# Optimization experiments

Hardware: AMD Instinct MI355X
Metric: run time of the kernel (lower is better)

## Reference

```python
import jax, jax.numpy as jnp
import numpy as np

H = 48; W = 48; WS = 8; NH = 12; FTH = 0.4; EPS = 1e-6


def _layernorm(x, w, b):
    mu = jnp.mean(x, axis=-1, keepdims=True)
    var = jnp.mean((x - mu) ** 2, axis=-1, keepdims=True)
    return (x - mu) * jax.lax.rsqrt(var + EPS) * w + b


def _mha(x, w_qkv, b_qkv, w_o, b_o, key_mask=None):
    # x: (Bn, N, C); w_qkv: (3, C, C); key_mask: (Bn, N) bool or None
    Bn, N, C = x.shape
    d = C // NH
    qkv = jnp.einsum('bnc,tcd->tbnd', x, w_qkv) + b_qkv[:, None, None, :]
    q, k, v = [t.reshape(Bn, N, NH, d).transpose(0, 2, 1, 3) for t in qkv]
    s = jnp.einsum('bhqd,bhkd->bhqk', q, k) / jnp.sqrt(jnp.asarray(d, x.dtype))
    if key_mask is not None:
        s = jnp.where(key_mask[:, None, None, :], s, jnp.asarray(-1e9, s.dtype))
    p = jax.nn.softmax(s, axis=-1)
    ctx = jnp.einsum('bhqk,bhkd->bhqd', p, v).transpose(0, 2, 1, 3).reshape(Bn, N, C)
    return ctx @ w_o + b_o


def _forward(x, mask, w_qkv_g, b_qkv_g, w_o_g, b_o_g, w_qkv_l, b_qkv_l, w_o_l, b_o_l,
             ln1_w, ln1_b, ln2_w, ln2_b, w_fc1, b_fc1, w_fc2, b_fc2):
    B, L, C = x.shape
    shortcut = x
    xn = _layernorm(x, ln1_w, ln1_b)

    # avg_pool2d(mask, 4, 4) -> (B, H, W); fg/bg split
    pooled = mask.reshape(B, 1, H, 4, W, 4).mean(axis=(3, 5))[:, 0]      # (B,H,W)
    fg = pooled > FTH                                                    # bool (B,H,W)
    fg_tok = fg.reshape(B, L)
    bg = (~fg).astype(x.dtype)
    # window-level bg mask: avg_pool(bg, WS) > 0 -> window contains any bg token
    bg_win = bg.reshape(B, H // WS, WS, W // WS, WS).mean(axis=(2, 4)) > 0.0   # (B, nH, nW)
    bg_win_tok = jnp.broadcast_to(bg_win[:, :, None, :, None],
                                  (B, H // WS, WS, W // WS, WS)).reshape(B, L)

    # local windowed attention on all windows (equivalent on bg windows; masked out elsewhere)
    xw = xn.reshape(B, H // WS, WS, W // WS, WS, C).transpose(0, 1, 3, 2, 4, 5)
    xw = xw.reshape(-1, WS * WS, C)                                      # (B*nWin, WS*WS, C)
    lout = _mha(xw, w_qkv_l, b_qkv_l, w_o_l, b_o_l)
    lout = lout.reshape(B, H // WS, W // WS, WS, WS, C).transpose(0, 1, 3, 2, 4, 5)
    lout = lout.reshape(B, L, C)

    # global attention with fg key mask (fg queries attend fg keys only)
    gout = _mha(xn, w_qkv_g, b_qkv_g, w_o_g, b_o_g, key_mask=fg_tok)

    # scatter-back semantics: fg positions take global output; bg-window positions take local output; rest zero
    zero = jnp.zeros((), x.dtype)
    x_new = jnp.where(fg_tok[..., None], gout,
                      jnp.where(bg_win_tok[..., None], lout, zero))

    x1 = shortcut + x_new
    h = _layernorm(x1, ln2_w, ln2_b)
    h = jax.nn.gelu(h @ w_fc1 + b_fc1, approximate=False) @ w_fc2 + b_fc2
    return x1 + h


def setup_inputs() -> dict:
    key = jax.random.key(0)
    ks = jax.random.split(key, 8)
    B, L, C, M = 2, H * W, 768, 3072
    s = 0.02
    return {
        'x': jax.random.normal(ks[0], (B, L, C), jnp.float32),
        'mask': jax.random.uniform(ks[1], (B, 1, 4 * H, 4 * W), jnp.float32),
        'w_qkv_g': jax.random.normal(ks[2], (3, C, C), jnp.float32) * s,
        'b_qkv_g': jnp.zeros((3, C), jnp.float32),
        'w_o_g': jax.random.normal(ks[3], (C, C), jnp.float32) * s,
        'b_o_g': jnp.zeros((C,), jnp.float32),
        'w_qkv_l': jax.random.normal(ks[4], (3, C, C), jnp.float32) * s,
        'b_qkv_l': jnp.zeros((3, C), jnp.float32),
        'w_o_l': jax.random.normal(ks[5], (C, C), jnp.float32) * s,
        'b_o_l': jnp.zeros((C,), jnp.float32),
        'ln1_w': jnp.ones((C,), jnp.float32),
        'ln1_b': jnp.zeros((C,), jnp.float32),
        'ln2_w': jnp.ones((C,), jnp.float32),
        'ln2_b': jnp.zeros((C,), jnp.float32),
        'w_fc1': jax.random.normal(ks[6], (C, M), jnp.float32) * s,
        'b_fc1': jnp.zeros((M,), jnp.float32),
        'w_fc2': jax.random.normal(ks[7], (M, C), jnp.float32) * s,
        'b_fc2': jnp.zeros((C,), jnp.float32),
    }


def reference(x, mask, w_qkv_g, b_qkv_g, w_o_g, b_o_g, w_qkv_l, b_qkv_l, w_o_l, b_o_l,
              ln1_w, ln1_b, ln2_w, ln2_b, w_fc1, b_fc1, w_fc2, b_fc2):
    return _forward(x, mask, w_qkv_g, b_qkv_g, w_o_g, b_o_g, w_qkv_l, b_qkv_l, w_o_l, b_o_l,
                    ln1_w, ln1_b, ln2_w, ln2_b, w_fc1, b_fc1, w_fc2, b_fc2)
```

## Files before the change

### kernel.cpp

```cpp
#include <hip/hip_runtime.h>
#include <math.h>

#define Lh 2304
#define Ch 768
#define NHh 12
#define Bh 2
#define QS2 3072

typedef unsigned short ushort_t;
typedef unsigned int uint_t;
typedef __attribute__((ext_vector_type(8))) short bf16x8;
typedef __attribute__((ext_vector_type(4))) float f32x4;
#define MFMA16(a, b, c) __builtin_amdgcn_mfma_f32_16x16x32_bf16(a, b, c, 0, 0, 0)

#define SCL2 0.18033688f
#define MSK2 1.4426950e9f
#if __has_builtin(__builtin_amdgcn_exp2f)
#define EXP2F(x) __builtin_amdgcn_exp2f(x)
#else
#define EXP2F(x) exp2f(x)
#endif

__device__ __forceinline__ ushort_t f2bf(float f) {
    union { float f; uint_t u; } v; v.f = f;
    uint_t u = v.u + 0x7fffu + ((v.u >> 16) & 1u);
    return (ushort_t)(u >> 16);
}
__device__ __forceinline__ uint_t pack2bf(float a, float b) {
    return (uint_t)f2bf(a) | ((uint_t)f2bf(b) << 16);
}

__device__ __forceinline__ void llds16(ushort_t* dst, const ushort_t* src) {
    __builtin_amdgcn_global_load_lds(
        (__attribute__((address_space(1))) void*)(const_cast<ushort_t*>(src)),
        (__attribute__((address_space(3))) void*)dst, 16, 0, 0);
}

__device__ __forceinline__ void ln_body(const float* __restrict__ x, const float* __restrict__ w,
                                        const float* __restrict__ b, ushort_t* __restrict__ y,
                                        int row, float* red)
{
    int tid = threadIdx.x;
    const float* xr = x + (size_t)row * Ch;
    float v0 = xr[tid], v1 = xr[tid + 256], v2 = xr[tid + 512];
    red[tid] = v0 + v1 + v2;
    __syncthreads();
    for (int st = 128; st > 0; st >>= 1) {
        if (tid < st) red[tid] += red[tid + st];
        __syncthreads();
    }
    float mean = red[0] * (1.0f / 768.0f);
    __syncthreads();
    float d0 = v0 - mean, d1 = v1 - mean, d2 = v2 - mean;
    red[tid] = d0 * d0 + d1 * d1 + d2 * d2;
    __syncthreads();
    for (int st = 128; st > 0; st >>= 1) {
        if (tid < st) red[tid] += red[tid + st];
        __syncthreads();
    }
    float rstd = rsqrtf(red[0] * (1.0f / 768.0f) + 1e-6f);
    ushort_t* yr = y + (size_t)row * Ch;
    yr[tid]       = f2bf(d0 * rstd * w[tid]       + b[tid]);
    yr[tid + 256] = f2bf(d1 * rstd * w[tid + 256] + b[tid + 256]);
    yr[tid + 512] = f2bf(d2 * rstd * w[tid + 512] + b[tid + 512]);
}

__global__ __launch_bounds__(256)
void layernorm_bf16_kernel(const float* __restrict__ x, const float* __restrict__ w,
                           const float* __restrict__ b, ushort_t* __restrict__ y)
{
    __shared__ float red[256];
    ln_body(x, w, b, y, blockIdx.x, red);
}

__global__ __launch_bounds__(256)
void ln_mask_kernel(const float* __restrict__ x, const float* __restrict__ w,
                    const float* __restrict__ b, ushort_t* __restrict__ y,
                    const float* __restrict__ mask, float* __restrict__ fg,
                    float* __restrict__ bgw)
{
    __shared__ float red[256];
    int bid = blockIdx.x;
    if (bid < 4608) {
        ln_body(x, w, b, y, bid, red);
        return;
    }
    int win = bid - 4608;
    int tid = threadIdx.x;
    if (tid >= 64) return;
    int bb = win / 36, ww = win % 36;
    int wi = ww / 6, wj = ww % 6;
    int i = wi * 8 + (tid >> 3), j = wj * 8 + (tid & 7);
    const float* mb = mask + (size_t)bb * 192 * 192 + (size_t)(i * 4) * 192 + j * 4;
    float s = 0.0f;
    #pragma unroll
    for (int di = 0; di < 4; ++di) {
        float4 v = *(const float4*)(mb + (size_t)di * 192);
        s += v.x + v.y + v.z + v.w;
    }
    float f = (s * (1.0f / 16.0f) > 0.4f) ? 1.0f : 0.0f;
    fg[bb * Lh + i * 48 + j] = f;
    unsigned long long bg = __ballot(f == 0.0f);
    if (tid == 0) bgw[win] = bg ? 1.0f : 0.0f;
}

__global__ __launch_bounds__(256)
void transpose_all_kernel(const float* __restrict__ w_qkv_g, const float* __restrict__ w_qkv_l,
                          const float* __restrict__ w_o_g, const float* __restrict__ w_o_l,
                          const float* __restrict__ w_fc1, const float* __restrict__ w_fc2,
                          const float* __restrict__ b_qkv_g, const float* __restrict__ b_qkv_l,
                          ushort_t* __restrict__ wtq, ushort_t* __restrict__ wt_o_g,
                          ushort_t* __restrict__ wt_o_l, ushort_t* __restrict__ wt_fc1,
                          ushort_t* __restrict__ wt_fc2, float* __restrict__ biasq)
{
    int blk = blockIdx.x;
    int tid = threadIdx.x;
    if (blk >= 2304) {
        int which = blk - 2304;
        const float* src = which ? b_qkv_l : b_qkv_g;
        float* dst = biasq + which * 2304;
        for (int i = tid; i < 2304; i += 256) dst[i] = src[i];
        return;
    }
    const float* W; ushort_t* D; int K, N, nx, bx;
    const size_t CC = (size_t)Ch * Ch;
    if (blk < 432)       { int t = blk / 144; bx = blk % 144;
                           W = w_qkv_g + t * CC; D = wtq + t * CC; K = 768; N = 768; nx = 12; }
    else if (blk < 864)  { int r = blk - 432; int t = r / 144; bx = r % 144;
                           W = w_qkv_l + t * CC; D = wtq + (size_t)2304 * 768 + t * CC;
                           K = 768; N = 768; nx = 12; }
    else if (blk < 1008) { bx = blk - 864;  W = w_o_g; D = wt_o_g; K = 768; N = 768; nx = 12; }
    else if (blk < 1152) { bx = blk - 1008; W = w_o_l; D = wt_o_l; K = 768; N = 768; nx = 12; }
    else if (blk < 1728) { bx = blk - 1152; W = w_fc1; D = wt_fc1; K = 768; N = 3072; nx = 48; }
    else                 { bx = blk - 1728; W = w_fc2; D = wt_fc2; K = 3072; N = 768; nx = 12; }
    int n0 = (bx % nx) * 64;
    int k0 = (bx / nx) * 64;
    __shared__ float T[64][65];
    #pragma unroll
    for (int i = 0; i < 16; ++i) {
        int lin = i * 256 + tid;
        int r = lin >> 6, c = lin & 63;
        T[r][c] = W[(size_t)(k0 + r) * N + n0 + c];
    }
    __syncthreads();
    #pragma unroll
    for (int i = 0; i < 4; ++i) {
        int lin = i * 256 + tid;
        int r = lin >> 4, c0 = (lin & 15) * 4;
        uint_t lo = pack2bf(T[c0][r], T[c0 + 1][r]);
        uint_t hi = pack2bf(T[c0 + 2][r], T[c0 + 3][r]);
        *(uint2*)&D[(size_t)(n0 + r) * K + k0 + c0] = make_uint2(lo, hi);
    }
}

template<int BNt, int VMODE>
__global__ __launch_bounds__(256)
void gemm_bf16_t(const ushort_t* __restrict__ A, const ushort_t* __restrict__ Bt,
                 const float* __restrict__ bias, const float* __restrict__ residual,
                 void* __restrict__ C, ushort_t* __restrict__ vt,
                 int M, int N, int K, int flags)
{
    __shared__ ushort_t AsL[2][128 * 32];
    __shared__ ushort_t BsL[2][BNt * 32];
    int bm = blockIdx.y * 128;
    int bx = blockIdx.x;
    int bn;
    if (VMODE == 1) {
        bn = (bx < 6) ? 1536 + bx * 128 : 3840 + (bx - 6) * 128;
    } else if (flags & 4) {
        bn = (bx < 12) ? bx * 128 : 2304 + (bx - 12) * 128;
    } else {
        bn = bx * BNt;
    }
    int tid = threadIdx.x;
    int lane = tid & 63;
    int wave = tid >> 6;
    int wm = wave >> 1, wn = wave & 1;
    int quad = lane >> 4, l15 = lane & 15;
    constexpr int NJ = BNt / 32;

    int srow = lane >> 2;
    int sg8 = ((lane & 3) ^ ((lane >> 3) & 3)) * 8;
    int fsw = (l15 >> 1) & 3;

    f32x4 acc[4][NJ];
    #pragma unroll
    for (int i = 0; i < 4; ++i)
        #pragma unroll
        for (int j = 0; j < NJ; ++j)
            acc[i][j] = (f32x4){0.f, 0.f, 0.f, 0.f};

    int iters = K / 32;
    llds16(&AsL[0][wave * 512], A + (size_t)(bm + wave * 16 + srow) * K + sg8);
    llds16(&AsL[0][(wave + 4) * 512], A + (size_t)(bm + (wave + 4) * 16 + srow) * K + sg8);
    llds16(&BsL[0][wave * 512], Bt + (size_t)(bn + wave * 16 + srow) * K + sg8);
    if (BNt == 128)
        llds16(&BsL[0][(wave + 4) * 512], Bt + (size_t)(bn + (wave + 4) * 16 + srow) * K + sg8);

    for (int kt = 0; kt < iters; ++kt) {
        int cur = kt & 1;
        __syncthreads();

        bf16x8 af[4], bfr[NJ];
        #pragma unroll
        for (int i = 0; i < 4; ++i)
            af[i] = *(const bf16x8*)&AsL[cur][(wm * 64 + i * 16 + l15) * 32 + ((quad ^ fsw) * 8)];
        #pragma unroll
        for (int j = 0; j < NJ; ++j)
            bfr[j] = *(const bf16x8*)&BsL[cur][(wn * (BNt / 2) + j * 16 + l15) * 32 + ((quad ^ fsw) * 8)];

        if (kt + 1 < iters) {
            int k0 = (kt + 1) * 32;
            int nxt = 1 - cur;
            llds16(&AsL[nxt][wave * 512], A + (size_t)(bm + wave * 16 + srow) * K + k0 + sg8);
            llds16(&AsL[nxt][(wave + 4) * 512], A + (size_t)(bm + (wave + 4) * 16 + srow) * K + k0 + sg8);
            llds16(&BsL[nxt][wave * 512], Bt + (size_t)(bn + wave * 16 + srow) * K + k0 + sg8);
            if (BNt == 128)
                llds16(&BsL[nxt][(wave + 4) * 512], Bt + (size_t)(bn + (wave + 4) * 16 + srow) * K + k0 + sg8);
        }

        if constexpr (VMODE == 0) {
            #pragma unroll
            for (int i = 0; i < 4; ++i)
                #pragma unroll
                for (int j = 0; j < NJ; ++j)
                    acc[i][j] = MFMA16(bfr[j], af[i], acc[i][j]);
        } else {
            #pragma unroll
            for (int i = 0; i < 4; ++i)
                #pragma unroll
                for (int j = 0; j < NJ; ++j)
                    acc[i][j] = MFMA16(af[i], bfr[j], acc[i][j]);
        }
    }

    if constexpr (VMODE == 1) {
        #pragma unroll
        for (int j = 0; j < NJ; ++j) {
            int col = bn + wn * (BNt / 2) + j * 16 + l15;
            int colp = col - ((col >= 3840) ? 3072 : 1536);
            float bc = bias[col];
            #pragma unroll
            for (int i = 0; i < 4; ++i) {
                int row0 = bm + wm * 64 + i * 16 + quad * 4;
                *(uint2*)&vt[(size_t)colp * 4608 + row0] =
                    make_uint2(pack2bf(acc[i][j][0] + bc, acc[i][j][1] + bc),
                               pack2bf(acc[i][j][2] + bc, acc[i][j][3] + bc));
            }
        }
        return;
    }

    #pragma unroll
    for (int i = 0; i < 4; ++i) {
        int row = bm + wm * 64 + i * 16 + l15;
        #pragma unroll
        for (int j = 0; j < NJ; ++j) {
            int col = bn + wn * (BNt / 2) + j * 16 + quad * 4;
            float4 bia = *(const float4*)&bias[col];
            float o0 = acc[i][j][0] + bia.x;
            float o1 = acc[i][j][1] + bia.y;
            float o2 = acc[i][j][2] + bia.z;
            float o3 = acc[i][j][3] + bia.w;
            if (flags & 1) {
                o0 = o0 * 0.5f * (1.0f + erff(o0 * 0.70710678f));
                o1 = o1 * 0.5f * (1.0f + erff(o1 * 0.70710678f));
                o2 = o2 * 0.5f * (1.0f + erff(o2 * 0.70710678f));
                o3 = o3 * 0.5f * (1.0f + erff(o3 * 0.70710678f));
            }
            if (residual) {
                float4 rs = *(const float4*)&residual[(size_t)row * N + col];
                o0 += rs.x; o1 += rs.y; o2 += rs.z; o3 += rs.w;
            }
            if (flags & 4) {
                int cq = col - ((col >= 2304) ? 768 : 0);
                *(uint2*)&((ushort_t*)C)[(size_t)row * QS2 + cq] =
                    make_uint2(pack2bf(o0, o1), pack2bf(o2, o3));
            } else if (flags & 2) {
                *(uint2*)&((ushort_t*)C)[(size_t)row * N + col] =
                    make_uint2(pack2bf(o0, o1), pack2bf(o2, o3));
            } else {
                *(float4*)&((float*)C)[(size_t)row * N + col] =
                    make_float4(o0, o1, o2, o3);
            }
        }
    }
}

__global__ __launch_bounds__(256)
void oproj_dual_kernel(const ushort_t* __restrict__ ctxg, const ushort_t* __restrict__ ctxl,
                       const ushort_t* __restrict__ Wg, const ushort_t* __restrict__ Wl,
                       const float* __restrict__ biasg, const float* __restrict__ biasl,
                       const float* __restrict__ x, float* __restrict__ x1,
                       const float* __restrict__ fg, const float* __restrict__ bgw)
{
    __shared__ ushort_t AgL[2][128 * 32];
    __shared__ ushort_t AlL[2][128 * 32];
    __shared__ ushort_t BgL[2][64 * 32];
    __shared__ ushort_t BlL[2][64 * 32];
    int bm = blockIdx.y * 128;
    int bn = blockIdx.x * 64;
    int tid = threadIdx.x;
    int lane = tid & 63;
    int wave = tid >> 6;
    int wm = wave >> 1, wn = wave & 1;
    int quad = lane >> 4, l15 = lane & 15;

    int srow = lane >> 2;
    int sg8 = ((lane & 3) ^ ((lane >> 3) & 3)) * 8;
    int fsw = (l15 >> 1) & 3;
    const int K = Ch, N = Ch, iters = Ch / 32;

    f32x4 accg[4][2], accl[4][2];
    #pragma unroll
    for (int i = 0; i < 4; ++i)
        #pragma unroll
        for (int j = 0; j < 2; ++j) {
            accg[i][j] = (f32x4){0.f, 0.f, 0.f, 0.f};
            accl[i][j] = (f32x4){0.f, 0.f, 0.f, 0.f};
        }

    llds16(&AgL[0][wave * 512], ctxg + (size_t)(bm + wave * 16 + srow) * K + sg8);
    llds16(&AgL[0][(wave + 4) * 512], ctxg + (size_t)(bm + (wave + 4) * 16 + srow) * K + sg8);
    llds16(&AlL[0][wave * 512], ctxl + (size_t)(bm + wave * 16 + srow) * K + sg8);
    llds16(&AlL[0][(wave + 4) * 512], ctxl + (size_t)(bm + (wave + 4) * 16 + srow) * K + sg8);
    llds16(&BgL[0][wave * 512], Wg + (size_t)(bn + wave * 16 + srow) * K + sg8);
    llds16(&BlL[0][wave * 512], Wl + (size_t)(bn + wave * 16 + srow) * K + sg8);

    for (int kt = 0; kt < iters; ++kt) {
        int cur = kt & 1;
        __syncthreads();
        bf16x8 afg[4], afl[4], bfg[2], bfl[2];
        #pragma unroll
        for (int i = 0; i < 4; ++i) {
            afg[i] = *(const bf16x8*)&AgL[cur][(wm * 64 + i * 16 + l15) * 32 + ((quad ^ fsw) * 8)];
            afl[i] = *(const bf16x8*)&AlL[cur][(wm * 64 + i * 16 + l15) * 32 + ((quad ^ fsw) * 8)];
        }
        #pragma unroll
        for (int j = 0; j < 2; ++j) {
            bfg[j] = *(const bf16x8*)&BgL[cur][(wn * 32 + j * 16 + l15) * 32 + ((quad ^ fsw) * 8)];
            bfl[j] = *(const bf16x8*)&BlL[cur][(wn * 32 + j * 16 + l15) * 32 + ((quad ^ fsw) * 8)];
        }
        if (kt + 1 < iters) {
            int k0 = (kt + 1) * 32;
            int nxt = 1 - cur;
            llds16(&AgL[nxt][wave * 512], ctxg + (size_t)(bm + wave * 16 + srow) * K + k0 + sg8);
            llds16(&AgL[nxt][(wave + 4) * 512], ctxg + (size_t)(bm + (wave + 4) * 16 + srow) * K + k0 + sg8);
            llds16(&AlL[nxt][wave * 512], ctxl + (size_t)(bm + wave * 16 + srow) * K + k0 + sg8);
            llds16(&AlL[nxt][(wave + 4) * 512], ctxl + (size_t)(bm + (wave + 4) * 16 + srow) * K + k0 + sg8);
            llds16(&BgL[nxt][wave * 512], Wg + (size_t)(bn + wave * 16 + srow) * K + k0 + sg8);
            llds16(&BlL[nxt][wave * 512], Wl + (size_t)(bn + wave * 16 + srow) * K + k0 + sg8);
        }
        #pragma unroll
        for (int i = 0; i < 4; ++i)
            #pragma unroll
            for (int j = 0; j < 2; ++j)
                accg[i][j] = MFMA16(bfg[j], afg[i], accg[i][j]);
        #pragma unroll
        for (int i = 0; i < 4; ++i)
            #pragma unroll
            for (int j = 0; j < 2; ++j)
                accl[i][j] = MFMA16(bfl[j], afl[i], accl[i][j]);
    }

    #pragma unroll
    for (int i = 0; i < 4; ++i) {
        int row = bm + wm * 64 + i * 16 + l15;
        int bb = (row >= Lh) ? 1 : 0;
        int n = row - bb * Lh;
        int ii = n / 48, jj = n % 48;
        float keepg = (fg[row] != 0.0f) ? 1.0f : 0.0f;
        float keepl = (keepg == 0.0f &&
                       bgw[bb * 36 + (ii >> 3) * 6 + (jj >> 3)] != 0.0f) ? 1.0f : 0.0f;
        #pragma unroll
        for (int j = 0; j < 2; ++j) {
            int col = bn + wn * 32 + j * 16 + quad * 4;
            float4 bg4 = *(const float4*)&biasg[col];
            float4 bl4 = *(const float4*)&biasl[col];
            float4 x4 = *(const float4*)&x[(size_t)row * N + col];
            float4 o;
            o.x = x4.x + keepg * (accg[i][j][0] + bg4.x) + keepl * (accl[i][j][0] + bl4.x);
            o.y = x4.y + keepg * (accg[i][j][1] + bg4.y) + keepl * (accl[i][j][1] + bl4.y);
            o.z = x4.z + keepg * (accg[i][j][2] + bg4.z) + keepl * (accl[i][j][2] + bl4.z);
            o.w = x4.w + keepg * (accg[i][j][3] + bg4.w) + keepl * (accl[i][j][3] + bl4.w);
            *(float4*)&x1[(size_t)row * N + col] = o;
        }
    }
}

__device__ __forceinline__ void attn_global_body(
    const ushort_t* __restrict__ QKV, const ushort_t* __restrict__ VT,
    const float* __restrict__ fg,
    float* __restrict__ Opart, float* __restrict__ Lpart,
    int tile, int h, int b, int half,
    ushort_t (*Ks)[2][64][32], ushort_t (*Vs)[2][64][32],
    ushort_t (*Ps)[72], float (*fgs)[64])
{
    int tid = threadIdx.x;
    int lane = tid & 63;
    int wave = tid >> 6;
    int quad = lane >> 4, l15 = lane & 15;
    int kb0 = half * 1152;

    bf16x8 aq[2][2];
    #pragma unroll
    for (int s = 0; s < 2; ++s) {
        int tok = tile * 128 + wave * 32 + s * 16 + l15;
        const ushort_t* qbase = QKV + (size_t)(b * Lh + tok) * QS2 + h * 64;
        #pragma unroll
        for (int step = 0; step < 2; ++step)
            aq[s][step] = *(const bf16x8*)(qbase + step * 32 + quad * 8);
    }

    int srow = lane >> 2;
    int sc = lane & 3;
    int krow = wave * 16 + srow;
    int scx = (sc ^ ((krow >> 1) & 3)) * 8;
    const ushort_t* ksrc = QKV + (size_t)(b * Lh + kb0 + krow) * QS2 + 768 + h * 64 + scx;
    const ushort_t* vsrc = VT + (size_t)(h * 64 + krow) * 4608 + b * Lh + kb0 + scx;

    float l_part[2] = {0.f, 0.f};
    f32x4 o_acc[2][4];
    #pragma unroll
    for (int s = 0; s < 2; ++s)
        #pragma unroll
        for (int t4 = 0; t4 < 4; ++t4) o_acc[s][t4] = (f32x4){0.f, 0.f, 0.f, 0.f};

    llds16(&Ks[0][0][wave * 16][0], ksrc);
    llds16(&Ks[0][1][wave * 16][0], ksrc + 32);
    llds16(&Vs[0][0][wave * 16][0], vsrc);
    llds16(&Vs[0][1][wave * 16][0], vsrc + 32);
    if (tid < 64) fgs[0][tid] = (fg[b * Lh + kb0 + tid] - 1.0f) * MSK2;

    int rfs = (l15 >> 1) & 3;

    for (int kt = 0; kt < 18; ++kt) {
        int cur = kt & 1, nxt = cur ^ 1;
        __syncthreads();

        bf16x8 bk[2][4];
        #pragma unroll
        for (int step = 0; step < 2; ++step)
            #pragma unroll
            for (int j4 = 0; j4 < 4; ++j4)
                bk[step][j4] = *(const bf16x8*)&Ks[cur][step][j4 * 16 + l15][(quad ^ rfs) * 8];

        if (kt + 1 < 18) {
            const ushort_t* kp = ksrc + (size_t)(kt + 1) * 64 * QS2;
            const ushort_t* vp = vsrc + (kt + 1) * 64;
            llds16(&Ks[nxt][0][wave * 16][0], kp);
            llds16(&Ks[nxt][1][wave * 16][0], kp + 32);
            llds16(&Vs[nxt][0][wave * 16][0], vp);
            llds16(&Vs[nxt][1][wave * 16][0], vp + 32);
            if (tid < 64) fgs[nxt][tid] = (fg[b * Lh + kb0 + (kt + 1) * 64 + tid] - 1.0f) * MSK2;
        }

        f32x4 s4[2][4];
        #pragma unroll
        for (int s = 0; s < 2; ++s)
            #pragma unroll
            for (int j4 = 0; j4 < 4; ++j4) s4[s][j4] = (f32x4){0.f, 0.f, 0.f, 0.f};
        __builtin_amdgcn_s_setprio(1);
        #pragma unroll
        for (int step = 0; step < 2; ++step)
            #pragma unroll
            for (int s = 0; s < 2; ++s)
                #pragma unroll
                for (int j4 = 0; j4 < 4; ++j4)
                    s4[s][j4] = MFMA16(bk[step][j4], aq[s][step], s4[s][j4]);
        __builtin_amdgcn_s_setprio(0);

        #pragma unroll
        for (int s = 0; s < 2; ++s) {
            int p0 = wave * 32 + s * 16;
            #pragma unroll
            for (int j4 = 0; j4 < 4; ++j4) {
                float4 mb4 = *(const float4*)&fgs[cur][j4 * 16 + quad * 4];
                float e0 = EXP2F(s4[s][j4][0] * SCL2 + mb4.x);
                float e1 = EXP2F(s4[s][j4][1] * SCL2 + mb4.y);
                float e2 = EXP2F(s4[s][j4][2] * SCL2 + mb4.z);
                float e3 = EXP2F(s4[s][j4][3] * SCL2 + mb4.w);
                l_part[s] += (e0 + e1) + (e2 + e3);
                uint_t a01 = __builtin_amdgcn_perm(__float_as_uint(e1), __float_as_uint(e0), 0x07060302u);
                uint_t a23 = __builtin_amdgcn_perm(__float_as_uint(e3), __float_as_uint(e2), 0x07060302u);
                *(uint2*)&Ps[p0 + l15][j4 * 16 + quad * 4] = make_uint2(a01, a23);
            }
        }
        #pragma unroll
        for (int step = 0; step < 2; ++step) {
            bf16x8 bv[4];
            #pragma unroll
            for (int t4 = 0; t4 < 4; ++t4)
                bv[t4] = *(const bf16x8*)&Vs[cur][step][t4 * 16 + l15][(quad ^ rfs) * 8];
            __builtin_amdgcn_s_setprio(1);
            #pragma unroll
            for (int s = 0; s < 2; ++s) {
                int p0 = wave * 32 + s * 16;
                bf16x8 a = *(const bf16x8*)&Ps[p0 + l15][step * 32 + quad * 8];
                #pragma unroll
                for (int t4 = 0; t4 < 4; ++t4)
                    o_acc[s][t4] = MFMA16(bv[t4], a, o_acc[s][t4]);
            }
            __builtin_amdgcn_s_setprio(0);
        }
    }

    #pragma unroll
    for (int s = 0; s < 2; ++s) {
        float v = l_part[s];
        v += __shfl_xor(v, 16, 64);
        v += __shfl_xor(v, 32, 64);
        int ql = wave * 32 + s * 16 + l15;
        int tok = tile * 128 + ql;
        float* op = Opart + ((size_t)half * 4608 + b * Lh + tok) * Ch + h * 64;
        #pragma unroll
        for (int t4 = 0; t4 < 4; ++t4)
            *(f32x4*)&op[t4 * 16 + quad * 4] = o_acc[s][t4];
        if (quad == 0)
            Lpart[((size_t)half * 4608 + b * Lh + tok) * NHh + h] = v;
    }
}

__device__ __forceinline__ void attn_local_body(
    const ushort_t* __restrict__ QKV, const ushort_t* __restrict__ VT,
    ushort_t* __restrict__ O, int tile, int h, int b,
    ushort_t (*Ks)[2][64][32], ushort_t (*Vs)[2][64][32], ushort_t (*Ps)[72])
{
    int tid = threadIdx.x;
    int lane = tid & 63;
    int wave = tid >> 6;
    int quad = lane >> 4, l15 = lane & 15;
    int wi = tile / 6, wj = tile % 6;

    bf16x8 aq[2];
    {
        int ql = wave * 16 + l15;
        int tok = (wi * 8 + (ql >> 3)) * 48 + wj * 8 + (ql & 7);
        const ushort_t* qbase = QKV + (size_t)(b * Lh + tok) * QS2 + 1536 + h * 64;
        #pragma unroll
        for (int step = 0; step < 2; ++step)
            aq[step] = *(const bf16x8*)(qbase + step * 32 + quad * 8);
    }

    {
        int srow = lane >> 2;
        int sc = lane & 3;
        int krow = wave * 16 + srow;
        int kfs = (krow >> 1) & 3;
        int tokK = (wi * 8 + (krow >> 3)) * 48 + wj * 8 + (krow & 7);
        const ushort_t* ksrc = QKV + (size_t)(b * Lh + tokK) * QS2 + 2304 + h * 64 + (sc ^ kfs) * 8;
        int c0 = sc ^ kfs;
        const ushort_t* vbase = VT + (size_t)(768 + h * 64 + krow) * 4608 + b * Lh + wj * 8;
        llds16(&Ks[0][0][wave * 16][0], ksrc);
        llds16(&Ks[0][1][wave * 16][0], ksrc + 32);
        llds16(&Vs[0][0][wave * 16][0], vbase + (wi * 8 + c0) * 48);
        llds16(&Vs[0][1][wave * 16][0], vbase + (wi * 8 + 4 + c0) * 48);
    }
    __syncthreads();

    float l_part = 0.f;
    f32x4 o_acc[4];
    #pragma unroll
    for (int t4 = 0; t4 < 4; ++t4) o_acc[t4] = (f32x4){0.f, 0.f, 0.f, 0.f};

    int rfs = (l15 >> 1) & 3;
    f32x4 s4[4];
    #pragma unroll
    for (int j4 = 0; j4 < 4; ++j4) s4[j4] = (f32x4){0.f, 0.f, 0.f, 0.f};
    #pragma unroll
    for (int step = 0; step < 2; ++step) {
        bf16x8 bk[4];
        #pragma unroll
        for (int j4 = 0; j4 < 4; ++j4)
            bk[j4] = *(const bf16x8*)&Ks[0][step][j4 * 16 + l15][(quad ^ rfs) * 8];
        #pragma unroll
        for (int j4 = 0; j4 < 4; ++j4)
            s4[j4] = MFMA16(bk[j4], aq[step], s4[j4]);
    }
    int p0 = wave * 16;
    #pragma unroll
    for (int j4 = 0; j4 < 4; ++j4) {
        float e0 = EXP2F(s4[j4][0] * SCL2);
        float e1 = EXP2F(s4[j4][1] * SCL2);
        float e2 = EXP2F(s4[j4][2] * SCL2);
        float e3 = EXP2F(s4[j4][3] * SCL2);
        l_part += (e0 + e1) + (e2 + e3);
        uint_t a01 = __builtin_amdgcn_perm(__float_as_uint(e1), __float_as_uint(e0), 0x07060302u);
        uint_t a23 = __builtin_amdgcn_perm(__float_as_uint(e3), __float_as_uint(e2), 0x07060302u);
        *(uint2*)&Ps[p0 + l15][j4 * 16 + quad * 4] = make_uint2(a01, a23);
    }
    #pragma unroll
    for (int step = 0; step < 2; ++step) {
        bf16x8 bv[4];
        #pragma unroll
        for (int t4 = 0; t4 < 4; ++t4)
            bv[t4] = *(const bf16x8*)&Vs[0][step][t4 * 16 + l15][(quad ^ rfs) * 8];
        bf16x8 a = *(const bf16x8*)&Ps[p0 + l15][step * 32 + quad * 8];
        #pragma unroll
        for (int t4 = 0; t4 < 4; ++t4)
            o_acc[t4] = MFMA16(bv[t4], a, o_acc[t4]);
    }

    {
        float v = l_part;
        v += __shfl_xor(v, 16, 64);
        v += __shfl_xor(v, 32, 64);
        float inv = 1.0f / v;
        int ql = wave * 16 + l15;
        int tok = (wi * 8 + (ql >> 3)) * 48 + wj * 8 + (ql & 7);
        ushort_t* ob = O + (size_t)(b * Lh + tok) * Ch + h * 64;
        #pragma unroll
        for (int t4 = 0; t4 < 4; ++t4) {
            *(uint2*)&ob[t4 * 16 + quad * 4] =
                make_uint2(pack2bf(o_acc[t4][0] * inv, o_acc[t4][1] * inv),
                           pack2bf(o_acc[t4][2] * inv, o_acc[t4][3] * inv));
        }
    }
}

__global__ __launch_bounds__(256)
void attn_fused_kernel(const ushort_t* __restrict__ QKV, const ushort_t* __restrict__ VT,
                       const float* __restrict__ fg,
                       float* __restrict__ Opart, float* __restrict__ Lpart,
                       ushort_t* __restrict__ ctxl)
{
    __shared__ __align__(16) ushort_t Ks[2][2][64][32];
    __shared__ __align__(16) ushort_t Vs[2][2][64][32];
    __shared__ __align__(16) ushort_t Ps[128][72];
    __shared__ float fgs[2][64];

    int bid = blockIdx.x;
    if (bid < 864) {
        int gid = (bid & 7) * 108 + (bid >> 3);
        int half = gid / 432;
        int rem = gid % 432;
        int tile = rem % 18;
        int h = (rem / 18) % NHh;
        int b = rem / 216;
        attn_global_body(QKV, VT, fg, Opart, Lpart, tile, h, b, half, Ks, Vs, Ps, fgs);
    } else {
        int rr = bid - 864;
        int lid = (rr & 7) * 108 + (rr >> 3);
        int tile = lid % 36;
        int h = (lid / 36) % NHh;
        int b = lid / 432;
        attn_local_body(QKV, VT, ctxl, tile, h, b, Ks, Vs, Ps);
    }
}

__global__ __launch_bounds__(192)
void attn_merge_kernel(const float* __restrict__ Op, const float* __restrict__ Lp,
                       ushort_t* __restrict__ ctxg)
{
    int r = blockIdx.x;
    int tid = threadIdx.x;
    int d = tid * 4;
    int h = d >> 6;
    float la = Lp[(size_t)r * NHh + h];
    float lb = Lp[((size_t)4608 + r) * NHh + h];
    float inv = 1.0f / (la + lb);
    const float* pa = Op + (size_t)r * Ch + d;
    const float* pb = Op + (size_t)4608 * Ch + (size_t)r * Ch + d;
    float4 a = *(const float4*)pa;
    float4 b4 = *(const float4*)pb;
    *(uint2*)&ctxg[(size_t)r * Ch + d] =
        make_uint2(pack2bf((a.x + b4.x) * inv, (a.y + b4.y) * inv),
                   pack2bf((a.z + b4.z) * inv, (a.w + b4.w) * inv));
}

extern "C" void kernel_launch(void* const* d_in, const int* in_sizes, int n_in,
                              void* d_out, int out_size, void* d_ws, size_t ws_size,
                              hipStream_t stream)
{
    const float* x       = (const float*)d_in[0];
    const float* mask    = (const float*)d_in[1];
    const float* w_qkv_g = (const float*)d_in[2];
    const float* b_qkv_g = (const float*)d_in[3];
    const float* w_o_g   = (const float*)d_in[4];
    const float* b_o_g   = (const float*)d_in[5];
    const float* w_qkv_l = (const float*)d_in[6];
    const float* b_qkv_l = (const float*)d_in[7];
    const float* w_o_l   = (const float*)d_in[8];
    const float* b_o_l   = (const float*)d_in[9];
    const float* ln1_w   = (const float*)d_in[10];
    const float* ln1_b   = (const float*)d_in[11];
    const float* ln2_w   = (const float*)d_in[12];
    const float* ln2_b   = (const float*)d_in[13];
    const float* w_fc1   = (const float*)d_in[14];
    const float* b_fc1   = (const float*)d_in[15];
    const float* w_fc2   = (const float*)d_in[16];
    const float* b_fc2   = (const float*)d_in[17];
    float* out = (float*)d_out;

    const size_t U = (size_t)Bh * Lh * Ch;
    char* p = (char*)d_ws;
    ushort_t* qkvb = (ushort_t*)p;        p += (size_t)4608 * 3072 * 2;
    ushort_t* vtb  = (ushort_t*)p;        p += (size_t)1536 * 4608 * 2;
    ushort_t* midb = qkvb;
    ushort_t* ctxg = (ushort_t*)p;        p += U * 2;
    ushort_t* ctxl = (ushort_t*)p;        p += U * 2;
    ushort_t* xnb  = (ushort_t*)p;        p += U * 2;
    float*    Opart = (float*)p;          p += (size_t)2 * U * 4;
    float*    Lpart = (float*)p;          p += (size_t)2 * 4608 * NHh * 4;
    float*    x1   = Opart;
    ushort_t* wtq  = (ushort_t*)p;        p += (size_t)4608 * 768 * 2;
    ushort_t* wt_o_g = (ushort_t*)p;      p += (size_t)768 * 768 * 2;
    ushort_t* wt_o_l = (ushort_t*)p;      p += (size_t)768 * 768 * 2;
    ushort_t* wt_fc1 = (ushort_t*)p;      p += (size_t)3072 * 768 * 2;
    ushort_t* wt_fc2 = (ushort_t*)p;      p += (size_t)768 * 3072 * 2;
    float*    biasq  = (float*)p;         p += 4608 * 4;
    float*    fg     = (float*)p;         p += Bh * Lh * 4;
    float*    bgw    = (float*)p;

    const int Mrows = Bh * Lh;
    dim3 blk(256);

    transpose_all_kernel<<<2306, blk, 0, stream>>>(
        w_qkv_g, w_qkv_l, w_o_g, w_o_l, w_fc1, w_fc2, b_qkv_g, b_qkv_l,
        wtq, wt_o_g, wt_o_l, wt_fc1, wt_fc2, biasq);

    ln_mask_kernel<<<4680, blk, 0, stream>>>(x, ln1_w, ln1_b, xnb, mask, fg, bgw);

    gemm_bf16_t<128, 0><<<dim3(24, Mrows / 128), blk, 0, stream>>>(
        xnb, wtq, biasq, nullptr, qkvb, nullptr, Mrows, 4608, Ch, 4);
    gemm_bf16_t<128, 1><<<dim3(12, Mrows / 128), blk, 0, stream>>>(
        xnb, wtq, biasq, nullptr, nullptr, vtb, Mrows, 4608, Ch, 4);

    attn_fused_kernel<<<1728, blk, 0, stream>>>(qkvb, vtb, fg, Opart, Lpart, ctxl);
    attn_merge_kernel<<<Mrows, dim3(192), 0, stream>>>(Opart, Lpart, ctxg);

    oproj_dual_kernel<<<dim3(Ch / 64, Mrows / 128), blk, 0, stream>>>(
        ctxg, ctxl, wt_o_g, wt_o_l, b_o_g, b_o_l, x, x1, fg, bgw);

    layernorm_bf16_kernel<<<Mrows, blk, 0, stream>>>(x1, ln2_w, ln2_b, xnb);

    gemm_bf16_t<128, 0><<<dim3(3072 / 128, Mrows / 128), blk, 0, stream>>>(
        xnb, wt_fc1, b_fc1, nullptr, midb, nullptr, Mrows, 3072, Ch, 1 | 2);
    gemm_bf16_t<64, 0><<<dim3(Ch / 64, Mrows / 128), blk, 0, stream>>>(
        midb, wt_fc2, b_fc2, x1, out, nullptr, Mrows, Ch, 3072, 0);
}
```

Before: 404.0 us.

## Switch global attention to 32x32 MFMA with register-resident P via permlane swap

Rewrites the global attention inner loop to use 32x32x16 bf16 MFMA tiles. The softmax probabilities now stay in registers: they are packed with v_cvt_pk_bf16_f32 and rearranged with v_permlane32_swap instead of going through an LDS round trip. The fg key mask is turned into a wave ballot bitmask, which drops the shared fg staging buffer. Shared memory is merged into one buffer with a new XOR swizzle, aiming to cut LDS traffic and instruction count, at the cost of more accumulator registers and reliance on gfx950-specific instructions.

```diff
diff --git a/kernel.cpp b/kernel.cpp
--- a/kernel.cpp
+++ b/kernel.cpp
@@ -11,7 +11,9 @@
 typedef unsigned int uint_t;
 typedef __attribute__((ext_vector_type(8))) short bf16x8;
 typedef __attribute__((ext_vector_type(4))) float f32x4;
+typedef __attribute__((ext_vector_type(16))) float f32x16;
 #define MFMA16(a, b, c) __builtin_amdgcn_mfma_f32_16x16x32_bf16(a, b, c, 0, 0, 0)
+#define MFMA32(a, b, c) __builtin_amdgcn_mfma_f32_32x32x16_bf16(a, b, c, 0, 0, 0)
 
 #define SCL2 0.18033688f
 #define MSK2 1.4426950e9f
@@ -28,6 +30,14 @@
 }
 __device__ __forceinline__ uint_t pack2bf(float a, float b) {
     return (uint_t)f2bf(a) | ((uint_t)f2bf(b) << 16);
+}
+__device__ __forceinline__ uint_t cvtpk(float lo, float hi) {
+    uint_t r;
+    asm("v_cvt_pk_bf16_f32 %0, %1, %2" : "=v"(r) : "v"(lo), "v"(hi));
+    return r;
+}
+__device__ __forceinline__ void plswap(uint_t& a, uint_t& b) {
+    asm volatile("v_permlane32_swap_b32 %0, %1" : "+v"(a), "+v"(b));
 }
 
 __device__ __forceinline__ void llds16(ushort_t* dst, const ushort_t* src) {
@@ -392,133 +402,120 @@
     const ushort_t* __restrict__ QKV, const ushort_t* __restrict__ VT,
     const float* __restrict__ fg,
     float* __restrict__ Opart, float* __restrict__ Lpart,
-    int tile, int h, int b, int half,
-    ushort_t (*Ks)[2][64][32], ushort_t (*Vs)[2][64][32],
-    ushort_t (*Ps)[72], float (*fgs)[64])
+    int tile, int h, int b, int half, ushort_t* SM)
 {
     int tid = threadIdx.x;
     int lane = tid & 63;
     int wave = tid >> 6;
-    int quad = lane >> 4, l15 = lane & 15;
+    int l31 = lane & 31;
+    int hi = lane >> 5;
     int kb0 = half * 1152;
 
-    bf16x8 aq[2][2];
-    #pragma unroll
-    for (int s = 0; s < 2; ++s) {
-        int tok = tile * 128 + wave * 32 + s * 16 + l15;
-        const ushort_t* qbase = QKV + (size_t)(b * Lh + tok) * QS2 + h * 64;
-        #pragma unroll
-        for (int step = 0; step < 2; ++step)
-            aq[s][step] = *(const bf16x8*)(qbase + step * 32 + quad * 8);
-    }
-
-    int srow = lane >> 2;
-    int sc = lane & 3;
-    int krow = wave * 16 + srow;
-    int scx = (sc ^ ((krow >> 1) & 3)) * 8;
-    const ushort_t* ksrc = QKV + (size_t)(b * Lh + kb0 + krow) * QS2 + 768 + h * 64 + scx;
-    const ushort_t* vsrc = VT + (size_t)(h * 64 + krow) * 4608 + b * Lh + kb0 + scx;
-
-    float l_part[2] = {0.f, 0.f};
-    f32x4 o_acc[2][4];
-    #pragma unroll
-    for (int s = 0; s < 2; ++s)
-        #pragma unroll
-        for (int t4 = 0; t4 < 4; ++t4) o_acc[s][t4] = (f32x4){0.f, 0.f, 0.f, 0.f};
-
-    llds16(&Ks[0][0][wave * 16][0], ksrc);
-    llds16(&Ks[0][1][wave * 16][0], ksrc + 32);
-    llds16(&Vs[0][0][wave * 16][0], vsrc);
-    llds16(&Vs[0][1][wave * 16][0], vsrc + 32);
-    if (tid < 64) fgs[0][tid] = (fg[b * Lh + kb0 + tid] - 1.0f) * MSK2;
-
-    int rfs = (l15 >> 1) & 3;
+    int tok_q = tile * 128 + wave * 32 + l31;
+    bf16x8 aq[4];
+    {
+        const ushort_t* qbase = QKV + (size_t)(b * Lh + tok_q) * QS2 + h * 64 + hi * 8;
+        #pragma unroll
+        for (int kkg = 0; kkg < 4; ++kkg)
+            aq[kkg] = *(const bf16x8*)(qbase + kkg * 16);
+    }
+
+    int srow = lane >> 3;
+    int schunk = (lane & 7) ^ srow;
+    int krow0 = wave * 16 + srow;
+    const ushort_t* ksrc  = QKV + (size_t)(b * Lh + kb0 + krow0) * QS2 + 768 + h * 64 + schunk * 8;
+    const ushort_t* ksrc2 = ksrc + (size_t)8 * QS2;
+    const ushort_t* vsrc  = VT + (size_t)(h * 64 + krow0) * 4608 + b * Lh + kb0 + schunk * 8;
+    const ushort_t* vsrc2 = vsrc + (size_t)8 * 4608;
+
+    ushort_t* KsB = SM;
+    ushort_t* VsB = SM + 8192;
+    int sdst = wave * 1024;
+
+    float l_part = 0.f;
+    f32x16 o_acc[2];
+    #pragma unroll
+    for (int dg = 0; dg < 2; ++dg)
+        #pragma unroll
+        for (int i = 0; i < 16; ++i) o_acc[dg][i] = 0.f;
+
+    llds16(KsB + sdst, ksrc);
+    llds16(KsB + sdst + 512, ksrc2);
+    llds16(VsB + sdst, vsrc);
+    llds16(VsB + sdst + 512, vsrc2);
+    float fgv = fg[b * Lh + kb0 + lane];
 
     for (int kt = 0; kt < 18; ++kt) {
         int cur = kt & 1, nxt = cur ^ 1;
         __syncthreads();
-
-        bf16x8 bk[2][4];
-        #pragma unroll
-        for (int step = 0; step < 2; ++step)
-            #pragma unroll
-            for (int j4 = 0; j4 < 4; ++j4)
-                bk[step][j4] = *(const bf16x8*)&Ks[cur][step][j4 * 16 + l15][(quad ^ rfs) * 8];
+        unsigned long long m64 = __ballot(fgv != 0.0f);
 
         if (kt + 1 < 18) {
-            const ushort_t* kp = ksrc + (size_t)(kt + 1) * 64 * QS2;
-            const ushort_t* vp = vsrc + (kt + 1) * 64;
-            llds16(&Ks[nxt][0][wave * 16][0], kp);
-            llds16(&Ks[nxt][1][wave * 16][0], kp + 32);
-            llds16(&Vs[nxt][0][wave * 16][0], vp);
-            llds16(&Vs[nxt][1][wave * 16][0], vp + 32);
-            if (tid < 64) fgs[nxt][tid] = (fg[b * Lh + kb0 + (kt + 1) * 64 + tid] - 1.0f) * MSK2;
-        }
-
-        f32x4 s4[2][4];
-        #pragma unroll
-        for (int s = 0; s < 2; ++s)
-            #pragma unroll
-            for (int j4 = 0; j4 < 4; ++j4) s4[s][j4] = (f32x4){0.f, 0.f, 0.f, 0.f};
-        __builtin_amdgcn_s_setprio(1);
-        #pragma unroll
-        for (int step = 0; step < 2; ++step)
-            #pragma unroll
-            for (int s = 0; s < 2; ++s)
+            const ushort_t* kp  = ksrc  + (size_t)(kt + 1) * 64 * QS2;
+            const ushort_t* kp2 = ksrc2 + (size_t)(kt + 1) * 64 * QS2;
+            llds16(KsB + nxt * 4096 + sdst, kp);
+            llds16(KsB + nxt * 4096 + sdst + 512, kp2);
+            llds16(VsB + nxt * 4096 + sdst, vsrc + (kt + 1) * 64);
+            llds16(VsB + nxt * 4096 + sdst + 512, vsrc2 + (kt + 1) * 64);
+            fgv = fg[b * Lh + kb0 + (kt + 1) * 64 + lane];
+        }
+
+        #pragma unroll
+        for (int kg = 0; kg < 2; ++kg) {
+            f32x16 sA;
+            #pragma unroll
+            for (int i = 0; i < 16; ++i) sA[i] = 0.f;
+            #pragma unroll
+            for (int kkg = 0; kkg < 4; ++kkg) {
+                bf16x8 bk = *(const bf16x8*)&KsB[cur * 4096 + (kg * 32 + l31) * 64 +
+                                                 (((kkg * 2 + hi) ^ (l31 & 7)) * 8)];
+                sA = MFMA32(bk, aq[kkg], sA);
+            }
+            float ev[16];
+            #pragma unroll
+            for (int r4 = 0; r4 < 4; ++r4) {
+                uint_t bits = (uint_t)(m64 >> (kg * 32 + 8 * r4 + 4 * hi)) & 0xFu;
                 #pragma unroll
-                for (int j4 = 0; j4 < 4; ++j4)
-                    s4[s][j4] = MFMA16(bk[step][j4], aq[s][step], s4[s][j4]);
-        __builtin_amdgcn_s_setprio(0);
-
-        #pragma unroll
-        for (int s = 0; s < 2; ++s) {
-            int p0 = wave * 32 + s * 16;
-            #pragma unroll
-            for (int j4 = 0; j4 < 4; ++j4) {
-                float4 mb4 = *(const float4*)&fgs[cur][j4 * 16 + quad * 4];
-                float e0 = EXP2F(s4[s][j4][0] * SCL2 + mb4.x);
-                float e1 = EXP2F(s4[s][j4][1] * SCL2 + mb4.y);
-                float e2 = EXP2F(s4[s][j4][2] * SCL2 + mb4.z);
-                float e3 = EXP2F(s4[s][j4][3] * SCL2 + mb4.w);
-                l_part[s] += (e0 + e1) + (e2 + e3);
-                uint_t a01 = __builtin_amdgcn_perm(__float_as_uint(e1), __float_as_uint(e0), 0x07060302u);
-                uint_t a23 = __builtin_amdgcn_perm(__float_as_uint(e3), __float_as_uint(e2), 0x07060302u);
-                *(uint2*)&Ps[p0 + l15][j4 * 16 + quad * 4] = make_uint2(a01, a23);
+                for (int s = 0; s < 4; ++s) {
+                    float m = (bits & (1u << s)) ? 0.0f : -MSK2;
+                    float e = EXP2F(sA[r4 * 4 + s] * SCL2 + m);
+                    ev[r4 * 4 + s] = e;
+                    l_part += e;
+                }
             }
-        }
-        #pragma unroll
-        for (int step = 0; step < 2; ++step) {
-            bf16x8 bv[4];
-            #pragma unroll
-            for (int t4 = 0; t4 < 4; ++t4)
-                bv[t4] = *(const bf16x8*)&Vs[cur][step][t4 * 16 + l15][(quad ^ rfs) * 8];
-            __builtin_amdgcn_s_setprio(1);
-            #pragma unroll
-            for (int s = 0; s < 2; ++s) {
-                int p0 = wave * 32 + s * 16;
-                bf16x8 a = *(const bf16x8*)&Ps[p0 + l15][step * 32 + quad * 8];
+            #pragma unroll
+            for (int th = 0; th < 2; ++th) {
+                int t16 = kg * 2 + th;
+                uint_t w0 = cvtpk(ev[8 * th + 0], ev[8 * th + 1]);
+                uint_t w1 = cvtpk(ev[8 * th + 2], ev[8 * th + 3]);
+                uint_t w2 = cvtpk(ev[8 * th + 4], ev[8 * th + 5]);
+                uint_t w3 = cvtpk(ev[8 * th + 6], ev[8 * th + 7]);
+                plswap(w0, w2);
+                plswap(w1, w3);
+                union { uint_t u[4]; bf16x8 v; } pw;
+                pw.u[0] = w0; pw.u[1] = w1; pw.u[2] = w2; pw.u[3] = w3;
                 #pragma unroll
-                for (int t4 = 0; t4 < 4; ++t4)
-                    o_acc[s][t4] = MFMA16(bv[t4], a, o_acc[s][t4]);
+                for (int dg = 0; dg < 2; ++dg) {
+                    bf16x8 bv = *(const bf16x8*)&VsB[cur * 4096 + (dg * 32 + l31) * 64 +
+                                                     (((t16 * 2 + hi) ^ (l31 & 7)) * 8)];
+                    o_acc[dg] = MFMA32(bv, pw.v, o_acc[dg]);
+                }
             }
-            __builtin_amdgcn_s_setprio(0);
-        }
-    }
-
-    #pragma unroll
-    for (int s = 0; s < 2; ++s) {
-        float v = l_part[s];
-        v += __shfl_xor(v, 16, 64);
-        v += __shfl_xor(v, 32, 64);
-        int ql = wave * 32 + s * 16 + l15;
-        int tok = tile * 128 + ql;
-        float* op = Opart + ((size_t)half * 4608 + b * Lh + tok) * Ch + h * 64;
-        #pragma unroll
-        for (int t4 = 0; t4 < 4; ++t4)
-            *(f32x4*)&op[t4 * 16 + quad * 4] = o_acc[s][t4];
-        if (quad == 0)
-            Lpart[((size_t)half * 4608 + b * Lh + tok) * NHh + h] = v;
-    }
+        }
+    }
+
+    float lsum = l_part + __shfl_xor(l_part, 32, 64);
+    float* op = Opart + ((size_t)half * 4608 + b * Lh + tok_q) * Ch + h * 64 + hi * 4;
+    #pragma unroll
+    for (int dg = 0; dg < 2; ++dg)
+        #pragma unroll
+        for (int r4 = 0; r4 < 4; ++r4) {
+            *(float4*)(op + dg * 32 + r4 * 8) =
+                make_float4(o_acc[dg][r4 * 4 + 0], o_acc[dg][r4 * 4 + 1],
+                            o_acc[dg][r4 * 4 + 2], o_acc[dg][r4 * 4 + 3]);
+        }
+    if (hi == 0)
+        Lpart[((size_t)half * 4608 + b * Lh + tok_q) * NHh + h] = lsum;
 }
 
 __device__ __forceinline__ void attn_local_body(
@@ -624,10 +621,7 @@
                        float* __restrict__ Opart, float* __restrict__ Lpart,
                        ushort_t* __restrict__ ctxl)
 {
-    __shared__ __align__(16) ushort_t Ks[2][2][64][32];
-    __shared__ __align__(16) ushort_t Vs[2][2][64][32];
-    __shared__ __align__(16) ushort_t Ps[128][72];
-    __shared__ float fgs[2][64];
+    __shared__ __align__(16) ushort_t SM[16384];
 
     int bid = blockIdx.x;
     if (bid < 864) {
@@ -637,14 +631,17 @@
         int tile = rem % 18;
         int h = (rem / 18) % NHh;
         int b = rem / 216;
-        attn_global_body(QKV, VT, fg, Opart, Lpart, tile, h, b, half, Ks, Vs, Ps, fgs);
+        attn_global_body(QKV, VT, fg, Opart, Lpart, tile, h, b, half, SM);
     } else {
         int rr = bid - 864;
         int lid = (rr & 7) * 108 + (rr >> 3);
         int tile = lid % 36;
         int h = (lid / 36) % NHh;
         int b = lid / 432;
-        attn_local_body(QKV, VT, ctxl, tile, h, b, Ks, Vs, Ps);
+        attn_local_body(QKV, VT, ctxl, tile, h, b,
+                        (ushort_t(*)[2][64][32])SM,
+                        (ushort_t(*)[2][64][32])(SM + 4096),
+                        (ushort_t(*)[72])(SM + 8192));
     }
 }
 
```

Result: no change. 408.9 us (+1.2%).
